# Optimization experiments

Hardware: AMD Instinct MI355X
Metric: run time of the kernel (lower is better)

Reference implementation:

```python
import jax, jax.numpy as jnp
import numpy as np

N, M, D = 8192, 8192, 256
GAMMA = 1.0 / D  # standard RBF bandwidth gamma = 1/D


def setup_inputs() -> dict:
    key = jax.random.key(0)
    kx, ks = jax.random.split(key)
    x = jax.random.normal(kx, (N, D), dtype=jnp.float32)
    support = jax.random.normal(ks, (M, D), dtype=jnp.float32)
    return {"x": x, "support": support}


def reference(x, support):
    # Vectorized RBF Gram matrix: K[i, j] = exp(-gamma * ||x_i - s_j||^2)
    # ||x_i - s_j||^2 = ||x_i||^2 + ||s_j||^2 - 2 x_i . s_j  (cdist-style, one GEMM)
    x_sq = jnp.sum(x * x, axis=-1, keepdims=True)            # [N, 1]
    s_sq = jnp.sum(support * support, axis=-1)[None, :]      # [1, M]
    cross = jnp.einsum('nd,md->nm', x, support)              # [N, M]
    sq_dists = jnp.maximum(x_sq + s_sq - 2.0 * cross, 0.0)   # clamp fp error
    return jnp.exp(-GAMMA * sq_dists)
```

## Files before the change

kernel.cpp:

```cpp
#include <hip/hip_runtime.h>

#define N 8192
#define M 8192
#define D 256

typedef unsigned short ushort_t;
typedef __attribute__((ext_vector_type(8))) short short8;
typedef __attribute__((ext_vector_type(4))) float floatx4;

__device__ __forceinline__ unsigned short f2bf(float f) {
  unsigned int u = __float_as_uint(f);
  u += 0x7fffu + ((u >> 16) & 1u);
  return (unsigned short)(u >> 16);
}

__global__ __launch_bounds__(256) void prep_kernel(const float* __restrict__ x,
                                                   const float* __restrict__ s,
                                                   ushort_t* __restrict__ xb,
                                                   ushort_t* __restrict__ sb,
                                                   float* __restrict__ xn,
                                                   float* __restrict__ sn) {
  int gw = blockIdx.x * 4 + (threadIdx.x >> 6);
  int lane = threadIdx.x & 63;
  const float* src;
  ushort_t* dst;
  float* nrm;
  int row;
  if (gw < N) { src = x; dst = xb; nrm = xn; row = gw; }
  else        { src = s; dst = sb; nrm = sn; row = gw - N; }
  float4 v = ((const float4*)(src + (size_t)row * D))[lane];
  float ss = v.x * v.x + v.y * v.y + v.z * v.z + v.w * v.w;
  ushort4 o;
  o.x = f2bf(v.x); o.y = f2bf(v.y); o.z = f2bf(v.z); o.w = f2bf(v.w);
  *(ushort4*)(dst + (size_t)row * D + lane * 4) = o;
#pragma unroll
  for (int off = 32; off > 0; off >>= 1) ss += __shfl_down(ss, off);
  if (lane == 0) nrm[row] = ss;
}

__global__ __launch_bounds__(256, 2) void rbf_gemm(const ushort_t* __restrict__ X,
                                                   const ushort_t* __restrict__ S,
                                                   const float* __restrict__ xn,
                                                   const float* __restrict__ sn,
                                                   float* __restrict__ out) {
  __shared__ __attribute__((aligned(16))) ushort_t As[4 * 128 * 32];
  __shared__ __attribute__((aligned(16))) ushort_t Bs[4 * 128 * 32];
  __shared__ float xnS[128];
  __shared__ float snS[128];

  const int tid = threadIdx.x;
  const int lane = tid & 63;
  const int wave = tid >> 6;
  const int bx = blockIdx.x;
  const int by = blockIdx.y;

  if (tid < 128) xnS[tid] = xn[by * 128 + tid];
  else           snS[tid - 128] = sn[bx * 128 + (tid - 128)];

  const int wr = (wave >> 1) * 64;
  const int wc = (wave & 1) * 64;

  const int srow = wave * 32 + (lane >> 2);
  const int scol = (lane & 3) * 8;
  const ushort_t* gA = X + (size_t)(by * 128 + srow) * D + scol;
  const ushort_t* gB = S + (size_t)(bx * 128 + srow) * D + scol;

  const int q4 = lane >> 4;
  const int m16 = lane & 15;

  floatx4 acc[4][4];
#pragma unroll
  for (int i = 0; i < 4; ++i)
#pragma unroll
    for (int j = 0; j < 4; ++j) acc[i][j] = (floatx4){0.f, 0.f, 0.f, 0.f};

#pragma unroll
  for (int r = 0; r < 2; ++r) {
    const int kb = r * 128;
    __syncthreads();
#pragma unroll
    for (int c = 0; c < 4; ++c) {
      const int k0 = kb + c * 32;
      ushort_t* lA = As + c * 4096 + wave * 1024;
      ushort_t* lB = Bs + c * 4096 + wave * 1024;
      __builtin_amdgcn_global_load_lds(
          (const __attribute__((address_space(1))) void*)(gA + k0),
          (__attribute__((address_space(3))) void*)(lA), 16, 0, 0);
      __builtin_amdgcn_global_load_lds(
          (const __attribute__((address_space(1))) void*)(gA + (size_t)16 * D + k0),
          (__attribute__((address_space(3))) void*)(lA + 512), 16, 0, 0);
      __builtin_amdgcn_global_load_lds(
          (const __attribute__((address_space(1))) void*)(gB + k0),
          (__attribute__((address_space(3))) void*)(lB), 16, 0, 0);
      __builtin_amdgcn_global_load_lds(
          (const __attribute__((address_space(1))) void*)(gB + (size_t)16 * D + k0),
          (__attribute__((address_space(3))) void*)(lB + 512), 16, 0, 0);
    }
    __syncthreads();

#pragma unroll
    for (int c = 0; c < 4; ++c) {
      const ushort_t* cA = As + c * 4096;
      const ushort_t* cB = Bs + c * 4096;
      short8 a_frag[4], b_frag[4];
#pragma unroll
      for (int i = 0; i < 4; ++i)
        a_frag[i] = *(const short8*)(cA + (wr + i * 16 + m16) * 32 + q4 * 8);
#pragma unroll
      for (int j = 0; j < 4; ++j)
        b_frag[j] = *(const short8*)(cB + (wc + j * 16 + m16) * 32 + q4 * 8);
#pragma unroll
      for (int i = 0; i < 4; ++i)
#pragma unroll
        for (int j = 0; j < 4; ++j)
          acc[i][j] = __builtin_amdgcn_mfma_f32_16x16x32_bf16(a_frag[i], b_frag[j],
                                                              acc[i][j], 0, 0, 0);
    }
  }

  const float cexp = -1.0f / (float)D;
#pragma unroll
  for (int i = 0; i < 4; ++i) {
#pragma unroll
    for (int j = 0; j < 4; ++j) {
#pragma unroll
      for (int r = 0; r < 4; ++r) {
        const int rl = wr + i * 16 + q4 * 4 + r;
        const int cl = wc + j * 16 + m16;
        float sq = xnS[rl] + snS[cl] - 2.0f * acc[i][j][r];
        sq = fmaxf(sq, 0.0f);
        out[(size_t)(by * 128 + rl) * M + (bx * 128 + cl)] = __expf(cexp * sq);
      }
    }
  }
}

extern "C" void kernel_launch(void* const* d_in, const int* in_sizes, int n_in,
                              void* d_out, int out_size, void* d_ws, size_t ws_size,
                              hipStream_t stream) {
  const float* x = (const float*)d_in[0];
  const float* s = (const float*)d_in[1];
  float* out = (float*)d_out;
  char* ws = (char*)d_ws;
  ushort_t* xb = (ushort_t*)ws;
  ushort_t* sb = (ushort_t*)(ws + (size_t)N * D * 2);
  float* xn = (float*)(ws + (size_t)(N + M) * D * 2);
  float* sn = xn + N;

  prep_kernel<<<(N + M) / 4, 256, 0, stream>>>(x, s, xb, sb, xn, sn);
  dim3 grid(M / 128, N / 128);
  rbf_gemm<<<grid, 256, 0, stream>>>(xb, sb, xn, sn, out);
}
```

Measured before the change: 294.4 us.

## Pre-tile bf16 operands with XOR swizzle and pipeline K-phase loads with staged waits

The prep kernel now writes bf16 operands in a tiled, XOR-swizzled layout, so each 128-row block is contiguous and LDS fragment reads avoid bank conflicts. The GEMM issues every global-to-LDS load for the full K=256 up front into a 128KB LDS buffer. It then computes four K-phases, each gated by a partial vmcnt wait, so compute overlaps the remaining loads. Blocks are also remapped through a grouped swizzle for L2 locality. The larger LDS footprint drops occupancy to one block per CU (launch_bounds 256,1), which could limit latency hiding in the store-heavy epilogue.

After: 320.5 us. 8.8% more time.

```diff
diff --git a/kernel.cpp b/kernel.cpp
--- a/kernel.cpp
+++ b/kernel.cpp
@@ -32,39 +32,88 @@
   float ss = v.x * v.x + v.y * v.y + v.z * v.z + v.w * v.w;
   ushort4 o;
   o.x = f2bf(v.x); o.y = f2bf(v.y); o.z = f2bf(v.z); o.w = f2bf(v.w);
-  *(ushort4*)(dst + (size_t)row * D + lane * 4) = o;
+  int lr = row & 127;
+  size_t off = (size_t)(row >> 7) * 65536 + (size_t)(lane >> 4) * 16384
+             + (size_t)lr * 128
+             + (size_t)(((((lane >> 1) & 7) ^ (lr & 7)) * 16) + (lane & 1) * 8);
+  *(ushort4*)((char*)dst + off) = o;
 #pragma unroll
-  for (int off = 32; off > 0; off >>= 1) ss += __shfl_down(ss, off);
+  for (int offs = 32; offs > 0; offs >>= 1) ss += __shfl_down(ss, offs);
   if (lane == 0) nrm[row] = ss;
 }
 
-__global__ __launch_bounds__(256, 2) void rbf_gemm(const ushort_t* __restrict__ X,
+template <int P>
+__device__ __forceinline__ void phase_compute(const ushort_t* As, const ushort_t* Bs,
+                                              floatx4 (&acc)[4][4], int wr, int wc,
+                                              int q4, int m16) {
+#pragma unroll
+  for (int cc = 0; cc < 2; ++cc) {
+    short8 a_frag[4], b_frag[4];
+#pragma unroll
+    for (int i = 0; i < 4; ++i) {
+      const int row = wr + i * 16 + m16;
+      a_frag[i] = *(const short8*)(As + P * 8192 + row * 64 +
+                                   (((cc * 4 + q4) ^ (row & 7)) << 3));
+    }
+#pragma unroll
+    for (int j = 0; j < 4; ++j) {
+      const int row = wc + j * 16 + m16;
+      b_frag[j] = *(const short8*)(Bs + P * 8192 + row * 64 +
+                                   (((cc * 4 + q4) ^ (row & 7)) << 3));
+    }
+#pragma unroll
+    for (int i = 0; i < 4; ++i)
+#pragma unroll
+      for (int j = 0; j < 4; ++j)
+        acc[i][j] = __builtin_amdgcn_mfma_f32_16x16x32_bf16(a_frag[i], b_frag[j],
+                                                            acc[i][j], 0, 0, 0);
+  }
+}
+
+__global__ __launch_bounds__(256, 1) void rbf_gemm(const ushort_t* __restrict__ X,
                                                    const ushort_t* __restrict__ S,
                                                    const float* __restrict__ xn,
                                                    const float* __restrict__ sn,
                                                    float* __restrict__ out) {
-  __shared__ __attribute__((aligned(16))) ushort_t As[4 * 128 * 32];
-  __shared__ __attribute__((aligned(16))) ushort_t Bs[4 * 128 * 32];
-  __shared__ float xnS[128];
-  __shared__ float snS[128];
+  __shared__ __attribute__((aligned(16))) ushort_t As[4 * 128 * 64];
+  __shared__ __attribute__((aligned(16))) ushort_t Bs[4 * 128 * 64];
+  __shared__ float nS[256];
 
   const int tid = threadIdx.x;
   const int lane = tid & 63;
   const int wave = tid >> 6;
-  const int bx = blockIdx.x;
-  const int by = blockIdx.y;
 
-  if (tid < 128) xnS[tid] = xn[by * 128 + tid];
-  else           snS[tid - 128] = sn[bx * 128 + (tid - 128)];
+  const int wg = blockIdx.y * 64 + blockIdx.x;
+  const int swz = (wg & 7) * 512 + (wg >> 3);
+  const int by = swz >> 6;
+  const int bx = swz & 63;
+
+  {
+    const float* np = (tid < 128) ? (xn + by * 128 + tid)
+                                  : (sn + bx * 128 + (tid - 128));
+    nS[tid] = *np;
+  }
+
+  const char* gA = (const char*)X + (size_t)by * 65536 + wave * 4096 + lane * 16;
+  const char* gB = (const char*)S + (size_t)bx * 65536 + wave * 4096 + lane * 16;
+  char* lA = (char*)As + wave * 4096;
+  char* lB = (char*)Bs + wave * 4096;
+#pragma unroll
+  for (int p = 0; p < 4; ++p) {
+#pragma unroll
+    for (int i = 0; i < 4; ++i)
+      __builtin_amdgcn_global_load_lds(
+          (const __attribute__((address_space(1))) void*)(gA + p * 16384 + i * 1024),
+          (__attribute__((address_space(3))) void*)(lA + p * 16384 + i * 1024), 16, 0, 0);
+#pragma unroll
+    for (int i = 0; i < 4; ++i)
+      __builtin_amdgcn_global_load_lds(
+          (const __attribute__((address_space(1))) void*)(gB + p * 16384 + i * 1024),
+          (__attribute__((address_space(3))) void*)(lB + p * 16384 + i * 1024), 16, 0, 0);
+  }
 
   const int wr = (wave >> 1) * 64;
   const int wc = (wave & 1) * 64;
-
-  const int srow = wave * 32 + (lane >> 2);
-  const int scol = (lane & 3) * 8;
-  const ushort_t* gA = X + (size_t)(by * 128 + srow) * D + scol;
-  const ushort_t* gB = S + (size_t)(bx * 128 + srow) * D + scol;
-
   const int q4 = lane >> 4;
   const int m16 = lane & 15;
 
@@ -74,49 +123,25 @@
 #pragma unroll
     for (int j = 0; j < 4; ++j) acc[i][j] = (floatx4){0.f, 0.f, 0.f, 0.f};
 
-#pragma unroll
-  for (int r = 0; r < 2; ++r) {
-    const int kb = r * 128;
-    __syncthreads();
-#pragma unroll
-    for (int c = 0; c < 4; ++c) {
-      const int k0 = kb + c * 32;
-      ushort_t* lA = As + c * 4096 + wave * 1024;
-      ushort_t* lB = Bs + c * 4096 + wave * 1024;
-      __builtin_amdgcn_global_load_lds(
-          (const __attribute__((address_space(1))) void*)(gA + k0),
-          (__attribute__((address_space(3))) void*)(lA), 16, 0, 0);
-      __builtin_amdgcn_global_load_lds(
-          (const __attribute__((address_space(1))) void*)(gA + (size_t)16 * D + k0),
-          (__attribute__((address_space(3))) void*)(lA + 512), 16, 0, 0);
-      __builtin_amdgcn_global_load_lds(
-          (const __attribute__((address_space(1))) void*)(gB + k0),
-          (__attribute__((address_space(3))) void*)(lB), 16, 0, 0);
-      __builtin_amdgcn_global_load_lds(
-          (const __attribute__((address_space(1))) void*)(gB + (size_t)16 * D + k0),
-          (__attribute__((address_space(3))) void*)(lB + 512), 16, 0, 0);
-    }
-    __syncthreads();
+  asm volatile("s_waitcnt vmcnt(24) lgkmcnt(0)" ::: "memory");
+  __builtin_amdgcn_s_barrier();
+  __builtin_amdgcn_sched_barrier(0);
+  phase_compute<0>(As, Bs, acc, wr, wc, q4, m16);
 
-#pragma unroll
-    for (int c = 0; c < 4; ++c) {
-      const ushort_t* cA = As + c * 4096;
-      const ushort_t* cB = Bs + c * 4096;
-      short8 a_frag[4], b_frag[4];
-#pragma unroll
-      for (int i = 0; i < 4; ++i)
-        a_frag[i] = *(const short8*)(cA + (wr + i * 16 + m16) * 32 + q4 * 8);
-#pragma unroll
-      for (int j = 0; j < 4; ++j)
-        b_frag[j] = *(const short8*)(cB + (wc + j * 16 + m16) * 32 + q4 * 8);
-#pragma unroll
-      for (int i = 0; i < 4; ++i)
-#pragma unroll
-        for (int j = 0; j < 4; ++j)
-          acc[i][j] = __builtin_amdgcn_mfma_f32_16x16x32_bf16(a_frag[i], b_frag[j],
-                                                              acc[i][j], 0, 0, 0);
-    }
-  }
+  asm volatile("s_waitcnt vmcnt(16)" ::: "memory");
+  __builtin_amdgcn_s_barrier();
+  __builtin_amdgcn_sched_barrier(0);
+  phase_compute<1>(As, Bs, acc, wr, wc, q4, m16);
+
+  asm volatile("s_waitcnt vmcnt(8)" ::: "memory");
+  __builtin_amdgcn_s_barrier();
+  __builtin_amdgcn_sched_barrier(0);
+  phase_compute<2>(As, Bs, acc, wr, wc, q4, m16);
+
+  asm volatile("s_waitcnt vmcnt(0)" ::: "memory");
+  __builtin_amdgcn_s_barrier();
+  __builtin_amdgcn_sched_barrier(0);
+  phase_compute<3>(As, Bs, acc, wr, wc, q4, m16);
 
   const float cexp = -1.0f / (float)D;
 #pragma unroll
@@ -127,7 +152,7 @@
       for (int r = 0; r < 4; ++r) {
         const int rl = wr + i * 16 + q4 * 4 + r;
         const int cl = wc + j * 16 + m16;
-        float sq = xnS[rl] + snS[cl] - 2.0f * acc[i][j][r];
+        float sq = nS[rl] + nS[128 + cl] - 2.0f * acc[i][j][r];
         sq = fmaxf(sq, 0.0f);
         out[(size_t)(by * 128 + rl) * M + (bx * 128 + cl)] = __expf(cexp * sq);
       }
```

## Pre-swizzle bf16 operands into MFMA fragment order for contiguous loads

Applied to the files above, without the earlier changes.

The prep kernel now writes the bf16 copies of x and support in a blocked layout that matches the MFMA fragment order, so each 16-row by 32-k sub-tile sits in a contiguous 1 KB chunk. The GEMM's global-to-LDS loads then become fully contiguous 1 KB transfers per wave. Fragment reads from LDS become lane-contiguous 16-byte reads, which should avoid bank conflicts from the previous row-stride-64B pattern. In exchange, the prep kernel's stores are scattered and the load/fragment index maths is tied to this specific layout.

After: 295.2 us. Within noise of the previous version (+0.3%).

```diff
diff --git a/kernel.cpp b/kernel.cpp
--- a/kernel.cpp
+++ b/kernel.cpp
@@ -32,9 +32,16 @@
   float ss = v.x * v.x + v.y * v.y + v.z * v.z + v.w * v.w;
   ushort4 o;
   o.x = f2bf(v.x); o.y = f2bf(v.y); o.z = f2bf(v.z); o.w = f2bf(v.w);
-  *(ushort4*)(dst + (size_t)row * D + lane * 4) = o;
+  const int g = row >> 6;
+  const int sub = (row >> 4) & 3;
+  const int m = row & 15;
+  const int c = lane >> 3;
+  const int q = (lane >> 1) & 3;
+  size_t off = (size_t)g * 32768 +
+               (size_t)((c * 4 + sub) * 1024 + q * 256 + m * 16 + (lane & 1) * 8);
+  *(ushort4*)((char*)dst + off) = o;
 #pragma unroll
-  for (int off = 32; off > 0; off >>= 1) ss += __shfl_down(ss, off);
+  for (int offs = 32; offs > 0; offs >>= 1) ss += __shfl_down(ss, offs);
   if (lane == 0) nrm[row] = ss;
 }
 
@@ -59,14 +66,13 @@
 
   const int wr = (wave >> 1) * 64;
   const int wc = (wave & 1) * 64;
-
-  const int srow = wave * 32 + (lane >> 2);
-  const int scol = (lane & 3) * 8;
-  const ushort_t* gA = X + (size_t)(by * 128 + srow) * D + scol;
-  const ushort_t* gB = S + (size_t)(bx * 128 + srow) * D + scol;
-
   const int q4 = lane >> 4;
   const int m16 = lane & 15;
+
+  const char* gAb = (const char*)X + (size_t)by * 65536 + lane * 16;
+  const char* gBb = (const char*)S + (size_t)bx * 65536 + lane * 16;
+  char* lAb = (char*)As + wave * 8192;
+  char* lBb = (char*)Bs + wave * 8192;
 
   floatx4 acc[4][4];
 #pragma unroll
@@ -76,39 +82,32 @@
 
 #pragma unroll
   for (int r = 0; r < 2; ++r) {
-    const int kb = r * 128;
+    const int kc4 = (r * 4 + wave) * 4;
     __syncthreads();
 #pragma unroll
-    for (int c = 0; c < 4; ++c) {
-      const int k0 = kb + c * 32;
-      ushort_t* lA = As + c * 4096 + wave * 1024;
-      ushort_t* lB = Bs + c * 4096 + wave * 1024;
+    for (int sub = 0; sub < 8; ++sub) {
+      const size_t gsel = (size_t)(sub >> 2) * 32768;
+      const int s4 = sub & 3;
       __builtin_amdgcn_global_load_lds(
-          (const __attribute__((address_space(1))) void*)(gA + k0),
-          (__attribute__((address_space(3))) void*)(lA), 16, 0, 0);
+          (const __attribute__((address_space(1))) void*)(gAb + gsel + ((kc4 + s4) << 10)),
+          (__attribute__((address_space(3))) void*)(lAb + (sub << 10)), 16, 0, 0);
       __builtin_amdgcn_global_load_lds(
-          (const __attribute__((address_space(1))) void*)(gA + (size_t)16 * D + k0),
-          (__attribute__((address_space(3))) void*)(lA + 512), 16, 0, 0);
-      __builtin_amdgcn_global_load_lds(
-          (const __attribute__((address_space(1))) void*)(gB + k0),
-          (__attribute__((address_space(3))) void*)(lB), 16, 0, 0);
-      __builtin_amdgcn_global_load_lds(
-          (const __attribute__((address_space(1))) void*)(gB + (size_t)16 * D + k0),
-          (__attribute__((address_space(3))) void*)(lB + 512), 16, 0, 0);
+          (const __attribute__((address_space(1))) void*)(gBb + gsel + ((kc4 + s4) << 10)),
+          (__attribute__((address_space(3))) void*)(lBb + (sub << 10)), 16, 0, 0);
     }
     __syncthreads();
 
 #pragma unroll
     for (int c = 0; c < 4; ++c) {
-      const ushort_t* cA = As + c * 4096;
-      const ushort_t* cB = Bs + c * 4096;
+      const char* cA = (const char*)As + c * 8192 + lane * 16;
+      const char* cB = (const char*)Bs + c * 8192 + lane * 16;
       short8 a_frag[4], b_frag[4];
 #pragma unroll
       for (int i = 0; i < 4; ++i)
-        a_frag[i] = *(const short8*)(cA + (wr + i * 16 + m16) * 32 + q4 * 8);
+        a_frag[i] = *(const short8*)(cA + ((wave >> 1) * 4 + i) * 1024);
 #pragma unroll
       for (int j = 0; j < 4; ++j)
-        b_frag[j] = *(const short8*)(cB + (wc + j * 16 + m16) * 32 + q4 * 8);
+        b_frag[j] = *(const short8*)(cB + ((wave & 1) * 4 + j) * 1024);
 #pragma unroll
       for (int i = 0; i < 4; ++i)
 #pragma unroll
```
